# Performance work log

Measured on AMD Instinct MI355X. Metric: run time of the kernel, lower is better.

The kernel has to match this reference:

```python
import jax, jax.numpy as jnp
import numpy as np

N_HEAD = 16
D_HEAD = 64
D_MODEL = 1024
LN_EPS = 1e-5


def layer_norm(x, gamma, beta):
    mu = jnp.mean(x, axis=-1, keepdims=True)
    var = jnp.mean((x - mu) ** 2, axis=-1, keepdims=True)
    return (x - mu) * jax.lax.rsqrt(var + LN_EPS) * gamma + beta


def setup_inputs() -> dict:
    key = jax.random.key(0)
    ks = jax.random.split(key, 6)
    B, T = 2, 2048
    inp = jax.random.normal(ks[0], (B, T, D_MODEL), dtype=jnp.float32)
    # qkv_net: Linear(d_model, 3*n_head*d_head)
    W_qkv = jax.random.normal(ks[1], (3 * N_HEAD * D_HEAD, D_MODEL), dtype=jnp.float32) * (D_MODEL ** -0.5)
    b_qkv = jax.random.normal(ks[2], (3 * N_HEAD * D_HEAD,), dtype=jnp.float32) * 0.02
    # o_net: Linear(n_head*d_head, d_model, bias=False)
    W_o = jax.random.normal(ks[3], (D_MODEL, N_HEAD * D_HEAD), dtype=jnp.float32) * ((N_HEAD * D_HEAD) ** -0.5)
    gamma = jnp.ones((D_MODEL,), dtype=jnp.float32)
    beta = jnp.zeros((D_MODEL,), dtype=jnp.float32)
    return {"inp": inp, "W_qkv": W_qkv, "b_qkv": b_qkv, "W_o": W_o, "gamma": gamma, "beta": beta}


def reference(inp, W_qkv, b_qkv, W_o, gamma, beta):
    B, T, D = inp.shape
    H, dh = N_HEAD, D_HEAD
    scale = 1.0 / (dh ** 0.5)

    qkv = inp @ W_qkv.T + b_qkv                      # (B, T, 3*H*dh)
    head_q, head_k, head_v = jnp.split(qkv, 3, axis=2)
    # (B, T, H, dh) -> (B, H, T, dh)
    q = head_q.reshape(B, T, H, dh).transpose(0, 2, 1, 3)
    k = head_k.reshape(B, T, H, dh).transpose(0, 2, 1, 3)
    v = head_v.reshape(B, T, H, dh).transpose(0, 2, 1, 3)

    attn_score = jnp.einsum('bhqd,bhkd->bhqk', q, k) * scale  # (B, H, T, T)
    attn_prob = jax.nn.softmax(attn_score, axis=-1)           # dropatt is identity in eval
    attn_vec = jnp.einsum('bhqk,bhkd->bhqd', attn_prob, v)    # (B, H, T, dh)

    # Faithful to original: (B*H, T, dh) batch-major buffer is VIEWED as (H, B, T, dh)
    attn_vec = attn_vec.reshape(H, B, T, dh)
    attn_vec = attn_vec.transpose(1, 2, 0, 3).reshape(B, T, H * dh)

    attn_out = attn_vec @ W_o.T                                # dropout identity in eval
    return layer_norm(inp + attn_out, gamma, beta)
```

## Files before the change

kernel.cpp:

```cpp
#include <hip/hip_runtime.h>
#include <hip/hip_bf16.h>
#include <stdint.h>

typedef __bf16 bf16_t;
typedef __bf16 bf16x8 __attribute__((ext_vector_type(8)));
typedef __bf16 bf16x4 __attribute__((ext_vector_type(4)));
typedef __bf16 bf16x2 __attribute__((ext_vector_type(2)));
typedef float floatx4 __attribute__((ext_vector_type(4)));

#define QSCALE 0.180336879f

#if __has_builtin(__builtin_amdgcn_cvt_pk_bf16_f32)
#define HAS_PK_BF16 1
#endif

__device__ static inline void gll16(const void* g, void* l) {
    __builtin_amdgcn_global_load_lds((const __attribute__((address_space(1))) void*)g,
                                     (__attribute__((address_space(3))) void*)l, 16, 0, 0);
}

__device__ static inline bf16x8 pack8(const float* p) {
    bf16x8 o;
#ifdef HAS_PK_BF16
#pragma unroll
    for (int j = 0; j < 4; j++) {
        bf16x2 t2 = __builtin_amdgcn_cvt_pk_bf16_f32(p[2 * j], p[2 * j + 1]);
        o[2 * j] = t2[0]; o[2 * j + 1] = t2[1];
    }
#else
#pragma unroll
    for (int j = 0; j < 8; j++) o[j] = (bf16_t)p[j];
#endif
    return o;
}

__global__ __launch_bounds__(256) void cvt_all(const float* __restrict__ inp,
                                               const float* __restrict__ wqkv,
                                               const float* __restrict__ wo,
                                               bf16_t* __restrict__ o_inp,
                                               bf16_t* __restrict__ o_wqkv,
                                               bf16_t* __restrict__ o_wo) {
    int blk = blockIdx.x;
    const float* src;
    bf16_t* dst;
    if (blk < 4096)      { src = inp;  dst = o_inp; }
    else if (blk < 7168) { src = wqkv; dst = o_wqkv; blk -= 4096; }
    else                 { src = wo;   dst = o_wo;   blk -= 7168; }
    int i = blk * 256 + threadIdx.x;
    float4 v = ((const float4*)src)[i];
    float p[4] = {v.x, v.y, v.z, v.w};
    bf16x4 o;
#ifdef HAS_PK_BF16
    bf16x2 t0 = __builtin_amdgcn_cvt_pk_bf16_f32(p[0], p[1]);
    bf16x2 t1 = __builtin_amdgcn_cvt_pk_bf16_f32(p[2], p[3]);
    o[0] = t0[0]; o[1] = t0[1]; o[2] = t1[0]; o[3] = t1[1];
#else
    o[0] = (bf16_t)p[0]; o[1] = (bf16_t)p[1]; o[2] = (bf16_t)p[2]; o[3] = (bf16_t)p[3];
#endif
    ((bf16x4*)dst)[i] = o;
}

__global__ __launch_bounds__(256, 3)
void gemm_qkv(const bf16_t* __restrict__ A, const bf16_t* __restrict__ Bw,
              const float* __restrict__ bias,
              bf16_t* __restrict__ qk, bf16_t* __restrict__ vT) {
    constexpr int K = 1024;
    __shared__ bf16_t lA[3][128 * 32];
    __shared__ bf16_t lB[3][128 * 32];
    const int tid  = threadIdx.x;
    const int lane = tid & 63, wave = tid >> 6;
    const int quad = lane >> 4, l16 = lane & 15;
    const int wy = wave >> 1, wx = wave & 1;

    const int L  = blockIdx.y * 24 + blockIdx.x;
    const int nL = (L & 7) * 96 + (L >> 3);
    const int bm = (nL / 24) * 128, bn = (nL % 24) * 128;

    const int c0 = tid, c1 = tid + 256;
    const int k0 = ((c0 & 3) ^ ((c0 >> 3) & 3)) * 8;
    const int k1 = ((c1 & 3) ^ ((c1 >> 3) & 3)) * 8;
    const bf16_t* Ap0 = A + (size_t)(bm + (c0 >> 2)) * K + k0;
    const bf16_t* Ap1 = A + (size_t)(bm + (c1 >> 2)) * K + k1;
    const bf16_t* Bp0 = Bw + (size_t)(bn + (c0 >> 2)) * K + k0;
    const bf16_t* Bp1 = Bw + (size_t)(bn + (c1 >> 2)) * K + k1;
    const int d0 = (wave * 64) * 8;
    const int d1 = (256 + wave * 64) * 8;

    const int sq8 = (quad ^ ((l16 >> 1) & 3)) * 8;

    floatx4 acc[4][4] = {};

    gll16(Ap0, &lA[0][d0]); gll16(Ap1, &lA[0][d1]);
    gll16(Bp0, &lB[0][d0]); gll16(Bp1, &lB[0][d1]);
    gll16(Ap0 + 32, &lA[1][d0]); gll16(Ap1 + 32, &lA[1][d1]);
    gll16(Bp0 + 32, &lB[1][d0]); gll16(Bp1 + 32, &lB[1][d1]);

    int cur = 0;
    for (int it = 0; it < 32; ++it) {
        if (it < 30) {
            const int kt = (it + 2) * 32;
            const int nb = cur >= 1 ? cur - 1 : 2;
            gll16(Ap0 + kt, &lA[nb][d0]); gll16(Ap1 + kt, &lA[nb][d1]);
            gll16(Bp0 + kt, &lB[nb][d0]); gll16(Bp1 + kt, &lB[nb][d1]);
            asm volatile("s_waitcnt vmcnt(8)" ::: "memory");
        } else if (it == 30) {
            asm volatile("s_waitcnt vmcnt(4)" ::: "memory");
        } else {
            asm volatile("s_waitcnt vmcnt(0)" ::: "memory");
        }
        __builtin_amdgcn_s_barrier();
        __builtin_amdgcn_sched_barrier(0);

        bf16x8 af[4], bfr[4];
#pragma unroll
        for (int i = 0; i < 4; i++) {
            af[i]  = *(const bf16x8*)(&lA[cur][(wy * 64 + i * 16 + l16) * 32 + sq8]);
            bfr[i] = *(const bf16x8*)(&lB[cur][(wx * 64 + i * 16 + l16) * 32 + sq8]);
        }
#pragma unroll
        for (int i = 0; i < 4; i++)
#pragma unroll
            for (int j = 0; j < 4; j++)
                acc[i][j] = __builtin_amdgcn_mfma_f32_16x16x32_bf16(af[i], bfr[j], acc[i][j], 0, 0, 0);

        __builtin_amdgcn_sched_barrier(0);
        __builtin_amdgcn_s_barrier();
        cur = cur < 2 ? cur + 1 : 0;
    }

    const bool is_v = (bn >= 2048);
#pragma unroll
    for (int j = 0; j < 4; j++) {
        const int n = bn + wx * 64 + j * 16 + l16;
        const float bv = bias[n];
        const bool isq = (n < 1024);
#pragma unroll
        for (int i = 0; i < 4; i++) {
            const int mbase = bm + wy * 64 + i * 16 + quad * 4;
            if (!is_v) {
#pragma unroll
                for (int r = 0; r < 4; r++) {
                    float c = acc[i][j][r] + bv;
                    if (isq) c *= QSCALE;
                    qk[(size_t)(mbase + r) * 2048 + n] = (bf16_t)c;
                }
            } else {
                const int nn = n - 2048;
                const int b  = mbase >> 11;
                const int t  = mbase & 2047;
                const int vrow = b * 1024 + nn;
                const int pcol = (t & ~31) | (((t >> 2) & 3) << 3) | (((t >> 4) & 1) << 2);
                bf16x4 pack;
#pragma unroll
                for (int r = 0; r < 4; r++) pack[r] = (bf16_t)(acc[i][j][r] + bv);
                *(bf16x4*)(vT + (size_t)vrow * 2048 + pcol) = pack;
            }
        }
    }
}

__global__ __launch_bounds__(256, 4)
void attn_kernel(const bf16_t* __restrict__ qk, const bf16_t* __restrict__ vT,
                 bf16_t* __restrict__ Opart, float* __restrict__ lpart) {
    __shared__ bf16_t Kbuf[2][64 * 64];
    __shared__ bf16_t Vbuf[2][64 * 64];
    const int tid  = threadIdx.x;
    const int lane = tid & 63, wave = tid >> 6;
    const int quad = lane >> 4, l16 = lane & 15;
    const int bid = blockIdx.x;
    const int s    = bid & 63;
    const int hl   = ((s & 7) << 2) | ((s >> 3) & 3);
    const int half = (s >> 5) & 1;
    const int qt   = bid >> 6;
    const int b = hl >> 4, h = hl & 15;
    const int kt0 = half * 1024;

    const bf16_t* Qbase = qk + (size_t)(b * 2048 + qt * 128 + wave * 32) * 2048 + h * 64;
    const bf16_t* Kbase = qk + (size_t)(b * 2048) * 2048 + 1024 + h * 64;
    const bf16_t* Vbase = vT + (size_t)(hl * 64) * 2048;

    const int srow = tid >> 2;
    const int sc8 = ((tid & 3) ^ ((tid >> 3) & 3)) * 8;
    const bf16_t* KgA = Kbase + (size_t)(kt0 + srow) * 2048 + sc8;
    const bf16_t* KgB = KgA + 32;
    const bf16_t* VgA = Vbase + (size_t)srow * 2048 + kt0 + sc8;
    const bf16_t* VgB = VgA + 32;
    const int wbase = wave * 512;

    const int xq8 = (quad ^ ((l16 >> 1) & 3)) * 8;

    bf16x8 qf[2][2];
#pragma unroll
    for (int rt = 0; rt < 2; rt++)
#pragma unroll
        for (int kc = 0; kc < 2; kc++)
            qf[rt][kc] = *(const bf16x8*)(Qbase + (size_t)(rt * 16 + l16) * 2048 + kc * 32 + quad * 8);

    floatx4 accO[2][4] = {};
    float lacc[2] = {0.f, 0.f};

    gll16(KgA, &Kbuf[0][wbase]);
    gll16(KgB, &Kbuf[0][2048 + wbase]);
    gll16(VgA, &Vbuf[0][wbase]);
    gll16(VgB, &Vbuf[0][2048 + wbase]);

    for (int it = 0; it < 16; ++it) {
        const int cur = it & 1, nxt = cur ^ 1;
        __syncthreads();
        if (it < 15) {
            const size_t ko = (size_t)(it + 1) * 64 * 2048;
            const int    vo = (it + 1) * 64;
            gll16(KgA + ko, &Kbuf[nxt][wbase]);
            gll16(KgB + ko, &Kbuf[nxt][2048 + wbase]);
            gll16(VgA + vo, &Vbuf[nxt][wbase]);
            gll16(VgB + vo, &Vbuf[nxt][2048 + wbase]);
        }
        floatx4 st[2][4] = {};
#pragma unroll
        for (int nt = 0; nt < 4; nt++) {
            bf16x8 k0 = *(const bf16x8*)&Kbuf[cur][(nt * 16 + l16) * 32 + xq8];
            bf16x8 k1 = *(const bf16x8*)&Kbuf[cur][2048 + (nt * 16 + l16) * 32 + xq8];
            st[0][nt] = __builtin_amdgcn_mfma_f32_16x16x32_bf16(k0, qf[0][0], st[0][nt], 0, 0, 0);
            st[0][nt] = __builtin_amdgcn_mfma_f32_16x16x32_bf16(k1, qf[0][1], st[0][nt], 0, 0, 0);
            st[1][nt] = __builtin_amdgcn_mfma_f32_16x16x32_bf16(k0, qf[1][0], st[1][nt], 0, 0, 0);
            st[1][nt] = __builtin_amdgcn_mfma_f32_16x16x32_bf16(k1, qf[1][1], st[1][nt], 0, 0, 0);
        }
#pragma unroll
        for (int kc2 = 0; kc2 < 2; kc2++) {
            bf16x8 vf[4];
#pragma unroll
            for (int ct = 0; ct < 4; ct++)
                vf[ct] = *(const bf16x8*)&Vbuf[cur][kc2 * 2048 + (ct * 16 + l16) * 32 + xq8];
#pragma unroll
            for (int rt = 0; rt < 2; rt++) {
                float p[8];
                float ls = 0.f;
#pragma unroll
                for (int j = 0; j < 8; j++) {
                    p[j] = __builtin_amdgcn_exp2f(st[rt][kc2 * 2 + (j >> 2)][j & 3]);
                    ls += p[j];
                }
                lacc[rt] += ls;
                bf16x8 pf = pack8(p);
#pragma unroll
                for (int ct = 0; ct < 4; ct++)
                    accO[rt][ct] = __builtin_amdgcn_mfma_f32_16x16x32_bf16(pf, vf[ct], accO[rt][ct], 0, 0, 0);
            }
        }
    }

    float lsum[2];
#pragma unroll
    for (int rt = 0; rt < 2; rt++) {
        float l = lacc[rt];
        l += __shfl_xor(l, 16);
        l += __shfl_xor(l, 32);
        lsum[rt] = l;
    }
    const int b2 = hl & 1;
    const int colb = hl >> 1;
    const int rowb = b2 * 2048 + qt * 128 + wave * 32;
    bf16_t* outb = Opart + (size_t)half * (4096 * 1024) + (size_t)rowb * 1024 + colb * 64;
#pragma unroll
    for (int rt = 0; rt < 2; rt++)
#pragma unroll
        for (int ct = 0; ct < 4; ct++)
#pragma unroll
            for (int r = 0; r < 4; r++)
                outb[(size_t)(rt * 16 + quad * 4 + r) * 1024 + ct * 16 + l16] = (bf16_t)(accO[rt][ct][r]);
    if (quad == 0) {
#pragma unroll
        for (int rt = 0; rt < 2; rt++)
            lpart[half * 65536 + (rowb + rt * 16 + l16) * 16 + colb] = lsum[rt];
    }
}

__global__ __launch_bounds__(256, 4)
void gemm_o(const bf16_t* __restrict__ Op, const float* __restrict__ lp,
            const bf16_t* __restrict__ Bw, bf16_t* __restrict__ out) {
    constexpr int K = 1024;
    __shared__ bf16_t lA[2][64 * 32];
    __shared__ bf16_t lB[2][128 * 32];
    const int tid  = threadIdx.x;
    const int lane = tid & 63, wave = tid >> 6;
    const int quad = lane >> 4, l16 = lane & 15;
    const int wy = wave >> 1, wx = wave & 1;
    const int bm = blockIdx.y * 64, bn = blockIdx.x * 128;

    const int ca = tid;
    const int arow = bm + (ca >> 2);
    const int ak   = (ca & 3) * 8;
    const int aslot = ((ca & 3) ^ ((ca >> 3) & 3));
    const int awr   = ((ca >> 2) * 4 + aslot) * 8;
    const bf16_t* Ap0 = Op + (size_t)arow * 1024 + ak;
    const bf16_t* Ap1 = Ap0 + (size_t)4096 * 1024;
    const float*  lrow = lp + arow * 16;
    const int cb0 = tid, cb1 = tid + 256;
    const int bk0 = ((cb0 & 3) ^ ((cb0 >> 3) & 3)) * 8;
    const int bk1 = ((cb1 & 3) ^ ((cb1 >> 3) & 3)) * 8;
    const bf16_t* Bp0 = Bw + (size_t)(bn + (cb0 >> 2)) * K + bk0;
    const bf16_t* Bp1 = Bw + (size_t)(bn + (cb1 >> 2)) * K + bk1;
    const int d0 = (wave * 64) * 8;
    const int d1 = (256 + wave * 64) * 8;

    const int xq8 = (quad ^ ((l16 >> 1) & 3)) * 8;

    gll16(Bp0, &lB[0][d0]);
    gll16(Bp1, &lB[0][d1]);
    {
        bf16x8 a0 = *(const bf16x8*)(Ap0);
        bf16x8 a1 = *(const bf16x8*)(Ap1);
        const float inv = 1.0f / (lrow[ak >> 6] + lrow[65536 + (ak >> 6)]);
        float p[8];
#pragma unroll
        for (int j = 0; j < 8; j++) p[j] = ((float)a0[j] + (float)a1[j]) * inv;
        *(bf16x8*)&lA[0][awr] = pack8(p);
    }

    floatx4 acc[2][4] = {};
    for (int it = 0; it < 32; ++it) {
        const int cur = it & 1, nxt = cur ^ 1;
        __syncthreads();
        bf16x8 na0, na1;
        int kt1 = (it + 1) * 32;
        if (it < 31) {
            na0 = *(const bf16x8*)(Ap0 + kt1);
            na1 = *(const bf16x8*)(Ap1 + kt1);
            gll16(Bp0 + kt1, &lB[nxt][d0]);
            gll16(Bp1 + kt1, &lB[nxt][d1]);
        }
        bf16x8 af[2], bfr[4];
#pragma unroll
        for (int i = 0; i < 2; i++)
            af[i] = *(const bf16x8*)(&lA[cur][(wy * 32 + i * 16 + l16) * 32 + xq8]);
#pragma unroll
        for (int j = 0; j < 4; j++)
            bfr[j] = *(const bf16x8*)(&lB[cur][(wx * 64 + j * 16 + l16) * 32 + xq8]);
#pragma unroll
        for (int i = 0; i < 2; i++)
#pragma unroll
            for (int j = 0; j < 4; j++)
                acc[i][j] = __builtin_amdgcn_mfma_f32_16x16x32_bf16(af[i], bfr[j], acc[i][j], 0, 0, 0);
        if (it < 31) {
            const int cb = (kt1 + ak) >> 6;
            const float inv = 1.0f / (lrow[cb] + lrow[65536 + cb]);
            float p[8];
#pragma unroll
            for (int j = 0; j < 8; j++) p[j] = ((float)na0[j] + (float)na1[j]) * inv;
            *(bf16x8*)&lA[nxt][awr] = pack8(p);
        }
    }
#pragma unroll
    for (int j = 0; j < 4; j++) {
        const int n = bn + wx * 64 + j * 16 + l16;
#pragma unroll
        for (int i = 0; i < 2; i++) {
            const int mbase = bm + wy * 32 + i * 16 + quad * 4;
#pragma unroll
            for (int r = 0; r < 4; r++)
                out[(size_t)(mbase + r) * 1024 + n] = (bf16_t)acc[i][j][r];
        }
    }
}

__global__ __launch_bounds__(256)
void ln_kernel(const float* __restrict__ inp, const bf16_t* __restrict__ ao,
               const float* __restrict__ gamma, const float* __restrict__ beta,
               float* __restrict__ out) {
    const int row = blockIdx.x, tid = threadIdx.x;
    const int wave = tid >> 6, lane = tid & 63;
    float4 a = ((const float4*)(inp + (size_t)row * 1024))[tid];
    bf16x4 c4 = ((const bf16x4*)(ao + (size_t)row * 1024))[tid];
    float x0 = a.x + (float)c4[0], x1 = a.y + (float)c4[1];
    float x2 = a.z + (float)c4[2], x3 = a.w + (float)c4[3];
    float s = x0 + x1 + x2 + x3;
    float sq = x0 * x0 + x1 * x1 + x2 * x2 + x3 * x3;
#pragma unroll
    for (int mm = 32; mm >= 1; mm >>= 1) {
        s += __shfl_xor(s, mm);
        sq += __shfl_xor(sq, mm);
    }
    __shared__ float rs[4], rq[4];
    if (lane == 0) { rs[wave] = s; rq[wave] = sq; }
    __syncthreads();
    s = rs[0] + rs[1] + rs[2] + rs[3];
    sq = rq[0] + rq[1] + rq[2] + rq[3];
    const float mu = s * (1.0f / 1024.0f);
    const float var = sq * (1.0f / 1024.0f) - mu * mu;
    const float rstd = rsqrtf(var + 1e-5f);
    float4 g = ((const float4*)gamma)[tid], bt = ((const float4*)beta)[tid];
    float4 o;
    o.x = (x0 - mu) * rstd * g.x + bt.x;
    o.y = (x1 - mu) * rstd * g.y + bt.y;
    o.z = (x2 - mu) * rstd * g.z + bt.z;
    o.w = (x3 - mu) * rstd * g.w + bt.w;
    ((float4*)(out + (size_t)row * 1024))[tid] = o;
}

extern "C" void kernel_launch(void* const* d_in, const int* in_sizes, int n_in,
                              void* d_out, int out_size, void* d_ws, size_t ws_size,
                              hipStream_t stream) {
    const float* inp   = (const float*)d_in[0];
    const float* Wqkv  = (const float*)d_in[1];
    const float* bqkv  = (const float*)d_in[2];
    const float* Wo    = (const float*)d_in[3];
    const float* gamma = (const float*)d_in[4];
    const float* beta  = (const float*)d_in[5];
    float* out = (float*)d_out;

    char* ws = (char*)d_ws;
    bf16_t* inp_bf  = (bf16_t*)(ws);
    bf16_t* wqkv_bf = (bf16_t*)(ws + (8u << 20));
    bf16_t* wo_bf   = (bf16_t*)(ws + (14u << 20));
    bf16_t* qk_buf  = (bf16_t*)(ws + (16u << 20));
    bf16_t* vT_buf  = (bf16_t*)(ws + (32u << 20));
    bf16_t* ao_bf   = (bf16_t*)(ws + (32u << 20));
    bf16_t* opart   = (bf16_t*)(ws + (48u << 20));
    float*  lpart   = (float*)(ws);

    cvt_all<<<8192, 256, 0, stream>>>(inp, Wqkv, Wo, inp_bf, wqkv_bf, wo_bf);
    gemm_qkv<<<dim3(24, 32), 256, 0, stream>>>(inp_bf, wqkv_bf, bqkv, qk_buf, vT_buf);
    attn_kernel<<<1024, 256, 0, stream>>>(qk_buf, vT_buf, opart, lpart);
    gemm_o<<<dim3(8, 64), 256, 0, stream>>>(opart, lpart, wo_bf, ao_bf);
    ln_kernel<<<4096, 256, 0, stream>>>(inp, ao_bf, gamma, beta, out);
}
```

Baseline: 202.1 us.

## Triple-buffer K/V tiles in attention with explicit vmcnt waits and MFMA priority

The attention kernel's K/V shared-memory staging goes from double to triple buffering, so loads are prefetched two iterations ahead. The compiler's full wait at __syncthreads is replaced with manual s_waitcnt vmcnt counts plus raw barriers, and MFMA sections are wrapped in s_setprio. The goal is to hide global-to-LDS load latency and keep the matrix units busy. The cost is 50% more LDS per block, which could reduce occupancy at 4 blocks per CU, and a second barrier per iteration.

```diff
diff --git a/kernel.cpp b/kernel.cpp
--- a/kernel.cpp
+++ b/kernel.cpp
@@ -162,8 +162,8 @@
 __global__ __launch_bounds__(256, 4)
 void attn_kernel(const bf16_t* __restrict__ qk, const bf16_t* __restrict__ vT,
                  bf16_t* __restrict__ Opart, float* __restrict__ lpart) {
-    __shared__ bf16_t Kbuf[2][64 * 64];
-    __shared__ bf16_t Vbuf[2][64 * 64];
+    __shared__ bf16_t Kbuf[3][64 * 64];
+    __shared__ bf16_t Vbuf[3][64 * 64];
     const int tid  = threadIdx.x;
     const int lane = tid & 63, wave = tid >> 6;
     const int quad = lane >> 4, l16 = lane & 15;
@@ -203,19 +203,35 @@
     gll16(KgB, &Kbuf[0][2048 + wbase]);
     gll16(VgA, &Vbuf[0][wbase]);
     gll16(VgB, &Vbuf[0][2048 + wbase]);
-
+    {
+        const size_t ko = (size_t)64 * 2048;
+        gll16(KgA + ko, &Kbuf[1][wbase]);
+        gll16(KgB + ko, &Kbuf[1][2048 + wbase]);
+        gll16(VgA + 64, &Vbuf[1][wbase]);
+        gll16(VgB + 64, &Vbuf[1][2048 + wbase]);
+    }
+
+    int cur = 0;
     for (int it = 0; it < 16; ++it) {
-        const int cur = it & 1, nxt = cur ^ 1;
-        __syncthreads();
-        if (it < 15) {
-            const size_t ko = (size_t)(it + 1) * 64 * 2048;
-            const int    vo = (it + 1) * 64;
-            gll16(KgA + ko, &Kbuf[nxt][wbase]);
-            gll16(KgB + ko, &Kbuf[nxt][2048 + wbase]);
-            gll16(VgA + vo, &Vbuf[nxt][wbase]);
-            gll16(VgB + vo, &Vbuf[nxt][2048 + wbase]);
-        }
+        if (it < 14) {
+            const int nb = cur >= 1 ? cur - 1 : 2;
+            const size_t ko = (size_t)(it + 2) * 64 * 2048;
+            const int    vo = (it + 2) * 64;
+            gll16(KgA + ko, &Kbuf[nb][wbase]);
+            gll16(KgB + ko, &Kbuf[nb][2048 + wbase]);
+            gll16(VgA + vo, &Vbuf[nb][wbase]);
+            gll16(VgB + vo, &Vbuf[nb][2048 + wbase]);
+            asm volatile("s_waitcnt vmcnt(8)" ::: "memory");
+        } else if (it == 14) {
+            asm volatile("s_waitcnt vmcnt(4)" ::: "memory");
+        } else {
+            asm volatile("s_waitcnt vmcnt(0)" ::: "memory");
+        }
+        __builtin_amdgcn_s_barrier();
+        __builtin_amdgcn_sched_barrier(0);
+
         floatx4 st[2][4] = {};
+        __builtin_amdgcn_s_setprio(1);
 #pragma unroll
         for (int nt = 0; nt < 4; nt++) {
             bf16x8 k0 = *(const bf16x8*)&Kbuf[cur][(nt * 16 + l16) * 32 + xq8];
@@ -225,6 +241,7 @@
             st[1][nt] = __builtin_amdgcn_mfma_f32_16x16x32_bf16(k0, qf[1][0], st[1][nt], 0, 0, 0);
             st[1][nt] = __builtin_amdgcn_mfma_f32_16x16x32_bf16(k1, qf[1][1], st[1][nt], 0, 0, 0);
         }
+        __builtin_amdgcn_s_setprio(0);
 #pragma unroll
         for (int kc2 = 0; kc2 < 2; kc2++) {
             bf16x8 vf[4];
@@ -242,11 +259,17 @@
                 }
                 lacc[rt] += ls;
                 bf16x8 pf = pack8(p);
+                __builtin_amdgcn_s_setprio(1);
 #pragma unroll
                 for (int ct = 0; ct < 4; ct++)
                     accO[rt][ct] = __builtin_amdgcn_mfma_f32_16x16x32_bf16(pf, vf[ct], accO[rt][ct], 0, 0, 0);
+                __builtin_amdgcn_s_setprio(0);
             }
         }
+
+        __builtin_amdgcn_sched_barrier(0);
+        __builtin_amdgcn_s_barrier();
+        cur = cur < 2 ? cur + 1 : 0;
     }
 
     float lsum[2];
```

After: 206.0 us. No clear change (+1.9%).

## Load K/V fragments directly from global memory instead of LDS double-buffering

Applied to the files above, without the earlier changes.

Removes the shared-memory double buffer for K and V tiles in the attention kernel. Each wave now loads its MFMA operand fragments straight from global memory (relying on L1/L2 for reuse across the four waves), which drops the __syncthreads barriers and LDS traffic. It also wraps the MFMA sequences in s_setprio to favour matrix work. The cost is that each wave issues four times the global loads with no prefetch overlap, so load latency is exposed inside the loop.

```diff
diff --git a/kernel.cpp b/kernel.cpp
--- a/kernel.cpp
+++ b/kernel.cpp
@@ -162,8 +162,6 @@
 __global__ __launch_bounds__(256, 4)
 void attn_kernel(const bf16_t* __restrict__ qk, const bf16_t* __restrict__ vT,
                  bf16_t* __restrict__ Opart, float* __restrict__ lpart) {
-    __shared__ bf16_t Kbuf[2][64 * 64];
-    __shared__ bf16_t Vbuf[2][64 * 64];
     const int tid  = threadIdx.x;
     const int lane = tid & 63, wave = tid >> 6;
     const int quad = lane >> 4, l16 = lane & 15;
@@ -176,18 +174,8 @@
     const int kt0 = half * 1024;
 
     const bf16_t* Qbase = qk + (size_t)(b * 2048 + qt * 128 + wave * 32) * 2048 + h * 64;
-    const bf16_t* Kbase = qk + (size_t)(b * 2048) * 2048 + 1024 + h * 64;
-    const bf16_t* Vbase = vT + (size_t)(hl * 64) * 2048;
-
-    const int srow = tid >> 2;
-    const int sc8 = ((tid & 3) ^ ((tid >> 3) & 3)) * 8;
-    const bf16_t* KgA = Kbase + (size_t)(kt0 + srow) * 2048 + sc8;
-    const bf16_t* KgB = KgA + 32;
-    const bf16_t* VgA = Vbase + (size_t)srow * 2048 + kt0 + sc8;
-    const bf16_t* VgB = VgA + 32;
-    const int wbase = wave * 512;
-
-    const int xq8 = (quad ^ ((l16 >> 1) & 3)) * 8;
+    const bf16_t* Kl = qk + (size_t)(b * 2048 + kt0 + l16) * 2048 + 1024 + h * 64 + quad * 8;
+    const bf16_t* Vl = vT + (size_t)(hl * 64 + l16) * 2048 + kt0 + quad * 8;
 
     bf16x8 qf[2][2];
 #pragma unroll
@@ -199,38 +187,31 @@
     floatx4 accO[2][4] = {};
     float lacc[2] = {0.f, 0.f};
 
-    gll16(KgA, &Kbuf[0][wbase]);
-    gll16(KgB, &Kbuf[0][2048 + wbase]);
-    gll16(VgA, &Vbuf[0][wbase]);
-    gll16(VgB, &Vbuf[0][2048 + wbase]);
-
     for (int it = 0; it < 16; ++it) {
-        const int cur = it & 1, nxt = cur ^ 1;
-        __syncthreads();
-        if (it < 15) {
-            const size_t ko = (size_t)(it + 1) * 64 * 2048;
-            const int    vo = (it + 1) * 64;
-            gll16(KgA + ko, &Kbuf[nxt][wbase]);
-            gll16(KgB + ko, &Kbuf[nxt][2048 + wbase]);
-            gll16(VgA + vo, &Vbuf[nxt][wbase]);
-            gll16(VgB + vo, &Vbuf[nxt][2048 + wbase]);
+        const bf16_t* Kit = Kl + (size_t)it * 64 * 2048;
+        const bf16_t* Vit = Vl + it * 64;
+        bf16x8 kf0[4], kf1[4];
+#pragma unroll
+        for (int nt = 0; nt < 4; nt++) {
+            kf0[nt] = *(const bf16x8*)(Kit + (size_t)(nt * 16) * 2048);
+            kf1[nt] = *(const bf16x8*)(Kit + (size_t)(nt * 16) * 2048 + 32);
         }
         floatx4 st[2][4] = {};
+        __builtin_amdgcn_s_setprio(1);
 #pragma unroll
         for (int nt = 0; nt < 4; nt++) {
-            bf16x8 k0 = *(const bf16x8*)&Kbuf[cur][(nt * 16 + l16) * 32 + xq8];
-            bf16x8 k1 = *(const bf16x8*)&Kbuf[cur][2048 + (nt * 16 + l16) * 32 + xq8];
-            st[0][nt] = __builtin_amdgcn_mfma_f32_16x16x32_bf16(k0, qf[0][0], st[0][nt], 0, 0, 0);
-            st[0][nt] = __builtin_amdgcn_mfma_f32_16x16x32_bf16(k1, qf[0][1], st[0][nt], 0, 0, 0);
-            st[1][nt] = __builtin_amdgcn_mfma_f32_16x16x32_bf16(k0, qf[1][0], st[1][nt], 0, 0, 0);
-            st[1][nt] = __builtin_amdgcn_mfma_f32_16x16x32_bf16(k1, qf[1][1], st[1][nt], 0, 0, 0);
-        }
+            st[0][nt] = __builtin_amdgcn_mfma_f32_16x16x32_bf16(kf0[nt], qf[0][0], st[0][nt], 0, 0, 0);
+            st[0][nt] = __builtin_amdgcn_mfma_f32_16x16x32_bf16(kf1[nt], qf[0][1], st[0][nt], 0, 0, 0);
+            st[1][nt] = __builtin_amdgcn_mfma_f32_16x16x32_bf16(kf0[nt], qf[1][0], st[1][nt], 0, 0, 0);
+            st[1][nt] = __builtin_amdgcn_mfma_f32_16x16x32_bf16(kf1[nt], qf[1][1], st[1][nt], 0, 0, 0);
+        }
+        __builtin_amdgcn_s_setprio(0);
 #pragma unroll
         for (int kc2 = 0; kc2 < 2; kc2++) {
             bf16x8 vf[4];
 #pragma unroll
             for (int ct = 0; ct < 4; ct++)
-                vf[ct] = *(const bf16x8*)&Vbuf[cur][kc2 * 2048 + (ct * 16 + l16) * 32 + xq8];
+                vf[ct] = *(const bf16x8*)(Vit + (size_t)(ct * 16) * 2048 + kc2 * 32);
 #pragma unroll
             for (int rt = 0; rt < 2; rt++) {
                 float p[8];
@@ -242,9 +223,11 @@
                 }
                 lacc[rt] += ls;
                 bf16x8 pf = pack8(p);
+                __builtin_amdgcn_s_setprio(1);
 #pragma unroll
                 for (int ct = 0; ct < 4; ct++)
                     accO[rt][ct] = __builtin_amdgcn_mfma_f32_16x16x32_bf16(pf, vf[ct], accO[rt][ct], 0, 0, 0);
+                __builtin_amdgcn_s_setprio(0);
             }
         }
     }
```

Measured after the change: 280.8 us. 1.39x slower.
